# Performance work log

Measured on AMD Instinct MI355X. Metric: run time of the kernel, lower is better.

The kernel has to match this reference:

```python
import jax, jax.numpy as jnp
import numpy as np

D = 1024
H = 16
DH = D // H


def setup_inputs() -> dict:
    key = jax.random.key(0)
    ks = jax.random.split(key, 9)
    s = 1.0 / np.sqrt(D)
    return {
        "x": jax.random.normal(ks[0], (4, 2048, D), dtype=jnp.float32),
        "wq": jax.random.uniform(ks[1], (D, D), jnp.float32, -s, s),
        "bq": jax.random.uniform(ks[2], (D,), jnp.float32, -s, s),
        "wk": jax.random.uniform(ks[3], (D, D), jnp.float32, -s, s),
        "bk": jax.random.uniform(ks[4], (D,), jnp.float32, -s, s),
        "wv": jax.random.uniform(ks[5], (D, D), jnp.float32, -s, s),
        "bv": jax.random.uniform(ks[6], (D,), jnp.float32, -s, s),
        "wo": jax.random.uniform(ks[7], (D, D), jnp.float32, -s, s),
        "bo": jax.random.uniform(ks[8], (D,), jnp.float32, -s, s),
    }


def reference(x, wq, bq, wk, bk, wv, bv, wo, bo):
    B, S, _ = x.shape
    # projections + split heads: [B, S, D] -> [B, H, S, Dh]
    def split(t):
        return t.reshape(B, S, H, DH).transpose(0, 2, 1, 3)
    q = split(x @ wq + bq)
    k = split(x @ wk + bk)
    v = split(x @ wv + bv)
    scale = 1.0 / jnp.sqrt(jnp.float32(DH))
    scores = jnp.einsum("bhqd,bhkd->bhqk", q, k) * scale  # [B,H,S,S]
    att = jax.nn.softmax(scores, axis=-1)
    out = jnp.einsum("bhqk,bhkd->bhqd", att, v)  # [B,H,S,Dh]
    out = out.transpose(0, 2, 1, 3).reshape(B, S, D)
    return out @ wo + bo
```

## Files before the change

### kernel.cpp

```cpp
#include <hip/hip_runtime.h>
#include <stdint.h>

typedef float f32x4 __attribute__((ext_vector_type(4)));
typedef __bf16 bf16x8 __attribute__((ext_vector_type(8)));
typedef unsigned short ushort_t;
typedef ushort_t ushortx8 __attribute__((ext_vector_type(8)));
typedef ushort_t ushortx4 __attribute__((ext_vector_type(4)));

#define DEV static __device__ __forceinline__

DEV ushort_t f2bf(float f) {
  union { float f; uint32_t u; } v; v.f = f;
  uint32_t u = v.u;
  return (ushort_t)((u + 0x7FFFu + ((u >> 16) & 1u)) >> 16);
}

DEV uint32_t pkbf(float a, float b) {
  __bf16 x = (__bf16)a, y = (__bf16)b;
  return (uint32_t)__builtin_bit_cast(unsigned short, x) |
         ((uint32_t)__builtin_bit_cast(unsigned short, y) << 16);
}

DEV void cp16(const void* g, void* l) {
  __builtin_amdgcn_global_load_lds((const __attribute__((address_space(1))) unsigned int*)g,
                                   (__attribute__((address_space(3))) unsigned int*)l,
                                   16, 0, 0);
}

DEV f32x4 mfma16(bf16x8 a, bf16x8 b, f32x4 c) {
  return __builtin_amdgcn_mfma_f32_16x16x32_bf16(a, b, c, 0, 0, 0);
}

__global__ __launch_bounds__(256) void k_prep(
    const float* __restrict__ x, ushort_t* __restrict__ xb,
    const float* __restrict__ wq, const float* __restrict__ wk,
    const float* __restrict__ wv, const float* __restrict__ wo,
    ushort_t* __restrict__ wqkvT, ushort_t* __restrict__ woT) {
  __shared__ float tile[32][33];
  int b = blockIdx.x;
  if (b < 4096) {
    size_t idx = ((size_t)b * 256 + threadIdx.x) * 8;
    const float4* src = (const float4*)(x + idx);
    float4 a = src[0], c = src[1];
    ushortx8 o;
    o[0] = f2bf(a.x); o[1] = f2bf(a.y); o[2] = f2bf(a.z); o[3] = f2bf(a.w);
    o[4] = f2bf(c.x); o[5] = f2bf(c.y); o[6] = f2bf(c.z); o[7] = f2bf(c.w);
    *(ushortx8*)(xb + idx) = o;
  } else {
    int t = b - 4096;
    int which = t >> 10;
    const float* src = (which == 0) ? wq : (which == 1) ? wk : (which == 2) ? wv : wo;
    ushort_t* dst = (which == 0) ? wqkvT
                    : (which == 1) ? wqkvT + 1024 * 1024
                    : (which == 2) ? wqkvT + 2 * 1024 * 1024
                                   : woT;
    int tt = t & 1023;
    int c0 = (tt & 31) * 32, r0 = (tt >> 5) * 32;
    int tx = threadIdx.x & 31, ty = threadIdx.x >> 5;
#pragma unroll
    for (int i = ty; i < 32; i += 8)
      tile[i][tx] = src[(size_t)(r0 + i) * 1024 + c0 + tx];
    __syncthreads();
#pragma unroll
    for (int i = ty; i < 32; i += 8)
      dst[(size_t)(c0 + i) * 1024 + r0 + tx] = f2bf(tile[tx][i]);
  }
}

__global__ __launch_bounds__(256) void k_transpose_v(const ushort_t* __restrict__ vw,
                                                     ushort_t* __restrict__ vtw) {
  __shared__ ushort_t t[64][72];
  int tid = threadIdx.x;
  int bh = blockIdx.y, s0 = blockIdx.x * 64;
#pragma unroll
  for (int n = 0; n < 2; ++n) {
    int row = (tid >> 3) + n * 32, ch = (tid & 7) * 8;
    *(ushortx8*)&t[row][ch] =
        *(const ushortx8*)&vw[((size_t)bh * 2048 + s0 + row) * 64 + ch];
  }
  __syncthreads();
#pragma unroll
  for (int n = 0; n < 2; ++n) {
    int dh = (tid >> 3) + n * 32, sc = (tid & 7) * 8;
    ushortx8 o;
#pragma unroll
    for (int k = 0; k < 8; ++k) o[k] = t[sc + k][dh];
    *(ushortx8*)&vtw[((size_t)bh * 64 + dh) * 2048 + s0 + sc] = o;
  }
}

template <int MODE>
__global__ __launch_bounds__(256, 2) void k_gemm(
    const ushort_t* __restrict__ A, const ushort_t* __restrict__ Bt,
    const float* __restrict__ b0, const float* __restrict__ b1,
    const float* __restrict__ b2, ushort_t* __restrict__ qw,
    ushort_t* __restrict__ kw, ushort_t* __restrict__ vw,
    float* __restrict__ outf) {
  const int K = 1024;
  __shared__ ushort_t As[128 * 32];
  __shared__ ushort_t Bs[128 * 32];
  int tid = threadIdx.x;
  int w = tid >> 6, lane = tid & 63, l16 = lane & 15, lg = lane >> 4;
  int m0 = blockIdx.x * 128, n0 = blockIdx.y * 128;
  int wm = (w >> 1) * 64, wn = (w & 1) * 64;
  f32x4 acc[4][4] = {};

  const ushort_t* Ag = A + (size_t)(m0 + (tid >> 2)) * K + (tid & 3) * 8;
  const ushort_t* Bg = Bt + (size_t)(n0 + (tid >> 2)) * K + (tid & 3) * 8;

  for (int k0 = 0; k0 < K; k0 += 32) {
    cp16(Ag + k0, As + w * 512);
    cp16(Ag + k0 + 64 * K, As + 2048 + w * 512);
    cp16(Bg + k0, Bs + w * 512);
    cp16(Bg + k0 + 64 * K, Bs + 2048 + w * 512);
    __syncthreads();
    bf16x8 af[4], bfr[4];
#pragma unroll
    for (int i = 0; i < 4; ++i)
      af[i] = *(const bf16x8*)&As[(wm + i * 16 + l16) * 32 + lg * 8];
#pragma unroll
    for (int j = 0; j < 4; ++j)
      bfr[j] = *(const bf16x8*)&Bs[(wn + j * 16 + l16) * 32 + lg * 8];
#pragma unroll
    for (int i = 0; i < 4; ++i)
#pragma unroll
      for (int j = 0; j < 4; ++j)
        acc[i][j] = mfma16(af[i], bfr[j], acc[i][j]);
    __syncthreads();
  }

  if (MODE == 0) {
    const float QSCALE = 0.18033688011112042f;
    int p = m0 >> 10;
    const float* bias = (p == 0) ? b0 : (p == 1) ? b1 : b2;
    ushort_t* dst = (p == 0) ? qw : (p == 1) ? kw : vw;
    float qs = (p == 0) ? QSCALE : 1.0f;
    int cbase = m0 & 1023;
#pragma unroll
    for (int i = 0; i < 4; ++i) {
      int oc = cbase + wm + i * 16 + lg * 4;
      int h = oc >> 6, dh0 = oc & 63;
      float4 bb = *(const float4*)&bias[oc];
#pragma unroll
      for (int j = 0; j < 4; ++j) {
        int tok = n0 + wn + j * 16 + l16;
        size_t base =
            ((size_t)((tok >> 11) * 16 + h) * 2048 + (tok & 2047)) * 64 + dh0;
        ushortx4 pk;
        pk[0] = f2bf((acc[i][j][0] + bb.x) * qs);
        pk[1] = f2bf((acc[i][j][1] + bb.y) * qs);
        pk[2] = f2bf((acc[i][j][2] + bb.z) * qs);
        pk[3] = f2bf((acc[i][j][3] + bb.w) * qs);
        *(ushortx4*)&dst[base] = pk;
      }
    }
  } else {
#pragma unroll
    for (int j = 0; j < 4; ++j) {
      int col = n0 + wn + j * 16 + l16;
      float bb = b0[col];
#pragma unroll
      for (int i = 0; i < 4; ++i) {
#pragma unroll
        for (int r = 0; r < 4; ++r) {
          int row = m0 + wm + i * 16 + lg * 4 + r;
          outf[(size_t)row * 1024 + col] = acc[i][j][r] + bb;
        }
      }
    }
  }
}

__global__ __launch_bounds__(512, 4) void k_attn(
    const ushort_t* __restrict__ qg, const ushort_t* __restrict__ kg,
    const ushort_t* __restrict__ vtg, ushort_t* __restrict__ att) {
  __shared__ ushort_t Ks[128 * 64];
  __shared__ ushort_t Vs[64 * 128];
  __shared__ ushort_t Ps[8][16 * 128];
  int tid = threadIdx.x;
  int w = tid >> 6, lane = tid & 63, l16 = lane & 15, lg = lane >> 4;
  int i = blockIdx.x;
  int bh = (i & 7) * 8 + ((i >> 3) & 7);
  int q0 = (i >> 6) * 256;
  const ushort_t* qh = qg + (size_t)bh * 2048 * 64;

  const ushort_t* kstage = kg + (size_t)bh * 2048 * 64 + (size_t)(tid >> 3) * 64 +
                           (size_t)(((tid & 7) ^ ((tid >> 3) & 7)) * 8);
  const ushort_t* vstage = vtg + (size_t)bh * 64 * 2048 + (size_t)(tid >> 4) * 2048 +
                           (size_t)(((tid & 15) ^ ((tid >> 4) & 15)) * 8);

  bf16x8 qf[2][2];
#pragma unroll
  for (int st = 0; st < 2; ++st)
#pragma unroll
    for (int ks = 0; ks < 2; ++ks)
      qf[st][ks] = *(const bf16x8*)(qh + (size_t)(q0 + w * 32 + st * 16 + l16) * 64 +
                                    ks * 32 + lg * 8);

  bf16x8 vone;
#pragma unroll
  for (int t = 0; t < 8; ++t) vone[t] = (__bf16)1.0f;

  f32x4 o[2][5] = {};

  for (int kb = 0; kb < 2048; kb += 128) {
    __syncthreads();
    cp16(kstage + (size_t)kb * 64, Ks + w * 512);
    cp16(kstage + (size_t)(kb + 64) * 64, Ks + 4096 + w * 512);
    cp16(vstage + kb, Vs + w * 512);
    cp16(vstage + kb + (size_t)32 * 2048, Vs + 4096 + w * 512);
    __syncthreads();

#pragma unroll
    for (int hf = 0; hf < 2; ++hf) {
      f32x4 sc[2][4] = {};
#pragma unroll
      for (int jt = 0; jt < 4; ++jt) {
        int row = hf * 64 + jt * 16 + l16;
        bf16x8 kf0 = *(const bf16x8*)&Ks[row * 64 + ((lg) ^ (l16 & 7)) * 8];
        bf16x8 kf1 = *(const bf16x8*)&Ks[row * 64 + ((lg + 4) ^ (l16 & 7)) * 8];
        sc[0][jt] = mfma16(kf0, qf[0][0], sc[0][jt]);
        sc[0][jt] = mfma16(kf1, qf[0][1], sc[0][jt]);
        sc[1][jt] = mfma16(kf0, qf[1][0], sc[1][jt]);
        sc[1][jt] = mfma16(kf1, qf[1][1], sc[1][jt]);
      }
#pragma unroll
      for (int st = 0; st < 2; ++st)
#pragma unroll
        for (int jt = 0; jt < 4; ++jt) {
          float e0 = __builtin_amdgcn_exp2f(sc[st][jt][0]);
          float e1 = __builtin_amdgcn_exp2f(sc[st][jt][1]);
          float e2 = __builtin_amdgcn_exp2f(sc[st][jt][2]);
          float e3 = __builtin_amdgcn_exp2f(sc[st][jt][3]);
          uint32_t* dst =
              (uint32_t*)&Ps[w][l16 * 128 +
                                (((st * 8 + jt * 2 + (lg >> 1)) ^ l16) * 8) +
                                (lg & 1) * 4];
          dst[0] = pkbf(e0, e1);
          dst[1] = pkbf(e2, e3);
        }
#pragma unroll
      for (int ks = 0; ks < 2; ++ks) {
        int kk = hf * 2 + ks;
        bf16x8 pf0 =
            *(const bf16x8*)&Ps[w][l16 * 128 + (((ks * 4 + lg) ^ l16) * 8)];
        bf16x8 pf1 =
            *(const bf16x8*)&Ps[w][l16 * 128 + (((8 + ks * 4 + lg) ^ l16) * 8)];
        o[0][4] = mfma16(pf0, vone, o[0][4]);
        o[1][4] = mfma16(pf1, vone, o[1][4]);
#pragma unroll
        for (int dt = 0; dt < 4; ++dt) {
          int vrow = dt * 16 + l16;
          bf16x8 vf =
              *(const bf16x8*)&Vs[vrow * 128 + (((kk * 4 + lg) ^ l16) * 8)];
          o[0][dt] = mfma16(pf0, vf, o[0][dt]);
          o[1][dt] = mfma16(pf1, vf, o[1][dt]);
        }
      }
    }
  }

  int bi = bh >> 4, h = bh & 15;
#pragma unroll
  for (int st = 0; st < 2; ++st) {
    f32x4 inv;
#pragma unroll
    for (int r = 0; r < 4; ++r) inv[r] = __builtin_amdgcn_rcpf(o[st][4][r]);
#pragma unroll
    for (int dt = 0; dt < 4; ++dt)
#pragma unroll
      for (int r = 0; r < 4; ++r) {
        int srow = q0 + w * 32 + st * 16 + lg * 4 + r;
        int col = h * 64 + dt * 16 + l16;
        att[(size_t)(bi * 2048 + srow) * 1024 + col] = f2bf(o[st][dt][r] * inv[r]);
      }
  }
}

extern "C" void kernel_launch(void* const* d_in, const int* in_sizes, int n_in,
                              void* d_out, int out_size, void* d_ws, size_t ws_size,
                              hipStream_t stream) {
  const float* x = (const float*)d_in[0];
  const float* wq = (const float*)d_in[1];
  const float* bq = (const float*)d_in[2];
  const float* wk = (const float*)d_in[3];
  const float* bk = (const float*)d_in[4];
  const float* wv = (const float*)d_in[5];
  const float* bv = (const float*)d_in[6];
  const float* wo = (const float*)d_in[7];
  const float* bo = (const float*)d_in[8];
  float* out = (float*)d_out;

  char* ws = (char*)d_ws;
  ushort_t* xb = (ushort_t*)(ws);
  ushort_t* wqkvT = (ushort_t*)(ws + 16777216);
  ushort_t* woT = (ushort_t*)(ws + 23068672);
  ushort_t* qw = (ushort_t*)(ws + 25165824);
  ushort_t* kw = (ushort_t*)(ws + 41943040);
  ushort_t* vtw = (ushort_t*)(ws + 58720256);
  ushort_t* att = (ushort_t*)(ws + 75497472);
  ushort_t* vw = att;

  k_prep<<<dim3(8192), dim3(256), 0, stream>>>(x, xb, wq, wk, wv, wo, wqkvT, woT);

  k_gemm<0><<<dim3(24, 64), dim3(256), 0, stream>>>(
      wqkvT, xb, bq, bk, bv, qw, kw, vw, nullptr);

  k_transpose_v<<<dim3(32, 64), dim3(256), 0, stream>>>(vw, vtw);

  k_attn<<<dim3(512), dim3(512), 0, stream>>>(qw, kw, vtw, att);

  k_gemm<1><<<dim3(64, 8), dim3(256), 0, stream>>>(
      att, woT, bo, nullptr, nullptr, nullptr, nullptr, nullptr, out);
}
```

Before: 294.0 us.

## Replace QKV projection GEMM with 256x256-tile double-buffered pipelined kernel

Adds a new QKV projection kernel that uses 256x256 tiles with 512 threads, 128KB of dynamic LDS holding double-buffered A/B stages, and XOR-swizzled LDS rows. Global-to-LDS copies for the next K slice are interleaved between MFMA phases, using explicit waitcnt, barriers and setprio. The goal is to raise arithmetic intensity and hide load latency compared with the old 128x128 single-buffer GEMM. The trade-off is only 384 blocks at low occupancy, plus a hipFuncSetAttribute call on every launch. The output GEMM is simplified to MODE 1 only.

```diff
diff --git a/kernel.cpp b/kernel.cpp
--- a/kernel.cpp
+++ b/kernel.cpp
@@ -89,13 +89,167 @@
   }
 }
 
+__global__ __launch_bounds__(512, 2) void k_gemm256(
+    const ushort_t* __restrict__ A, const ushort_t* __restrict__ Bt,
+    const float* __restrict__ b0, const float* __restrict__ b1,
+    const float* __restrict__ b2, ushort_t* __restrict__ qw,
+    ushort_t* __restrict__ kw, ushort_t* __restrict__ vw) {
+  extern __shared__ ushort_t lds[];
+  ushort_t* As = lds;
+  ushort_t* Bs = lds + 32768;
+  const int K = 1024, NT = 16;
+  int tid = threadIdx.x;
+  int w = tid >> 6, lane = tid & 63, l16 = lane & 15, lg = lane >> 4;
+  int wr = w >> 2, wc = w & 3;
+  int m0 = blockIdx.x * 256, n0 = blockIdx.y * 256;
+
+  const ushort_t* Asrc = A + (size_t)(m0 + w * 8 + (lane >> 3)) * K +
+                         (size_t)(((lane & 7) ^ (lane >> 3)) * 8);
+  const ushort_t* Bsrc = Bt + (size_t)(n0 + w * 8 + (lane >> 3)) * K +
+                         (size_t)(((lane & 7) ^ (lane >> 3)) * 8);
+
+  f32x4 acc[8][4] = {};
+  bf16x8 a[4][2], b[4][2];
+  const int aRow = wr * 128 + l16, bRow = wc * 64 + l16, rsw = l16 & 7;
+
+#pragma unroll
+  for (int s = 0; s < 4; ++s)
+    cp16(Asrc + (size_t)s * 64 * K, As + s * 4096 + w * 512);
+#pragma unroll
+  for (int s = 0; s < 4; ++s)
+    cp16(Bsrc + (size_t)s * 64 * K, Bs + s * 4096 + w * 512);
+  cp16(Asrc + 64, As + 16384 + w * 512);
+  cp16(Asrc + (size_t)65536 + 64, As + 16384 + 4096 + w * 512);
+  asm volatile("s_waitcnt vmcnt(2)" ::: "memory");
+  __builtin_amdgcn_s_barrier();
+
+  for (int t = 0; t < NT; ++t) {
+    int cur = t & 1, nxt = cur ^ 1;
+    ushort_t* AsC = As + cur * 16384;
+    ushort_t* BsC = Bs + cur * 16384;
+    ushort_t* AsN = As + nxt * 16384;
+    ushort_t* BsN = Bs + nxt * 16384;
+    const ushort_t* An = Asrc + (size_t)(t + 1) * 64;
+    const ushort_t* Bn = Bsrc + (size_t)(t + 1) * 64;
+
+#pragma unroll
+    for (int i2 = 0; i2 < 4; ++i2)
+#pragma unroll
+      for (int ks = 0; ks < 2; ++ks)
+        a[i2][ks] = *(const bf16x8*)&AsC[(aRow + i2 * 16) * 64 +
+                                         (((ks << 2) | lg) ^ rsw) * 8];
+#pragma unroll
+    for (int j2 = 0; j2 < 2; ++j2)
+#pragma unroll
+      for (int ks = 0; ks < 2; ++ks)
+        b[j2][ks] = *(const bf16x8*)&BsC[(bRow + j2 * 16) * 64 +
+                                         (((ks << 2) | lg) ^ rsw) * 8];
+    cp16(An + (size_t)2 * 65536, AsN + 2 * 4096 + w * 512);
+    cp16(An + (size_t)3 * 65536, AsN + 3 * 4096 + w * 512);
+    __builtin_amdgcn_s_barrier();
+    asm volatile("s_waitcnt lgkmcnt(0)" ::: "memory");
+    __builtin_amdgcn_s_setprio(1);
+#pragma unroll
+    for (int i2 = 0; i2 < 4; ++i2)
+#pragma unroll
+      for (int j2 = 0; j2 < 2; ++j2)
+#pragma unroll
+        for (int ks = 0; ks < 2; ++ks)
+          acc[i2][j2] = mfma16(a[i2][ks], b[j2][ks], acc[i2][j2]);
+    __builtin_amdgcn_s_setprio(0);
+    __builtin_amdgcn_s_barrier();
+
+#pragma unroll
+    for (int j2 = 2; j2 < 4; ++j2)
+#pragma unroll
+      for (int ks = 0; ks < 2; ++ks)
+        b[j2][ks] = *(const bf16x8*)&BsC[(bRow + j2 * 16) * 64 +
+                                         (((ks << 2) | lg) ^ rsw) * 8];
+    cp16(Bn, BsN + w * 512);
+    cp16(Bn + (size_t)65536, BsN + 4096 + w * 512);
+    __builtin_amdgcn_s_barrier();
+    asm volatile("s_waitcnt lgkmcnt(0)" ::: "memory");
+    __builtin_amdgcn_s_setprio(1);
+#pragma unroll
+    for (int i2 = 0; i2 < 4; ++i2)
+#pragma unroll
+      for (int j2 = 2; j2 < 4; ++j2)
+#pragma unroll
+        for (int ks = 0; ks < 2; ++ks)
+          acc[i2][j2] = mfma16(a[i2][ks], b[j2][ks], acc[i2][j2]);
+    __builtin_amdgcn_s_setprio(0);
+    __builtin_amdgcn_s_barrier();
+
+#pragma unroll
+    for (int i2 = 0; i2 < 4; ++i2)
+#pragma unroll
+      for (int ks = 0; ks < 2; ++ks)
+        a[i2][ks] = *(const bf16x8*)&AsC[(aRow + (4 + i2) * 16) * 64 +
+                                         (((ks << 2) | lg) ^ rsw) * 8];
+    cp16(Bn + (size_t)2 * 65536, BsN + 2 * 4096 + w * 512);
+    cp16(Bn + (size_t)3 * 65536, BsN + 3 * 4096 + w * 512);
+    __builtin_amdgcn_s_barrier();
+    asm volatile("s_waitcnt lgkmcnt(0)" ::: "memory");
+    __builtin_amdgcn_s_setprio(1);
+#pragma unroll
+    for (int i2 = 0; i2 < 4; ++i2)
+#pragma unroll
+      for (int j2 = 2; j2 < 4; ++j2)
+#pragma unroll
+        for (int ks = 0; ks < 2; ++ks)
+          acc[4 + i2][j2] = mfma16(a[i2][ks], b[j2][ks], acc[4 + i2][j2]);
+    __builtin_amdgcn_s_setprio(0);
+    __builtin_amdgcn_s_barrier();
+
+    {
+      const ushort_t* A2 = Asrc + (size_t)(t + 2) * 64;
+      cp16(A2, AsC + w * 512);
+      cp16(A2 + (size_t)65536, AsC + 4096 + w * 512);
+    }
+    asm volatile("s_waitcnt vmcnt(2)" ::: "memory");
+    __builtin_amdgcn_s_barrier();
+    __builtin_amdgcn_s_setprio(1);
+#pragma unroll
+    for (int i2 = 0; i2 < 4; ++i2)
+#pragma unroll
+      for (int j2 = 0; j2 < 2; ++j2)
+#pragma unroll
+        for (int ks = 0; ks < 2; ++ks)
+          acc[4 + i2][j2] = mfma16(a[i2][ks], b[j2][ks], acc[4 + i2][j2]);
+    __builtin_amdgcn_s_setprio(0);
+    __builtin_amdgcn_s_barrier();
+  }
+
+  const float QSCALE = 0.18033688011112042f;
+  int p = blockIdx.x >> 2;
+  const float* bias = (p == 0) ? b0 : (p == 1) ? b1 : b2;
+  ushort_t* dst = (p == 0) ? qw : (p == 1) ? kw : vw;
+  float qs = (p == 0) ? QSCALE : 1.0f;
+  int cbase = (m0 & 1023) + wr * 128;
+#pragma unroll
+  for (int i = 0; i < 8; ++i) {
+    int oc = cbase + i * 16 + lg * 4;
+    int h = oc >> 6, dh0 = oc & 63;
+    float4 bb = *(const float4*)&bias[oc];
+#pragma unroll
+    for (int j = 0; j < 4; ++j) {
+      int tok = n0 + wc * 64 + j * 16 + l16;
+      size_t base =
+          ((size_t)((tok >> 11) * 16 + h) * 2048 + (tok & 2047)) * 64 + dh0;
+      ushortx4 pk;
+      pk[0] = f2bf((acc[i][j][0] + bb.x) * qs);
+      pk[1] = f2bf((acc[i][j][1] + bb.y) * qs);
+      pk[2] = f2bf((acc[i][j][2] + bb.z) * qs);
+      pk[3] = f2bf((acc[i][j][3] + bb.w) * qs);
+      *(ushortx4*)&dst[base] = pk;
+    }
+  }
+}
+
 template <int MODE>
 __global__ __launch_bounds__(256, 2) void k_gemm(
     const ushort_t* __restrict__ A, const ushort_t* __restrict__ Bt,
-    const float* __restrict__ b0, const float* __restrict__ b1,
-    const float* __restrict__ b2, ushort_t* __restrict__ qw,
-    ushort_t* __restrict__ kw, ushort_t* __restrict__ vw,
-    float* __restrict__ outf) {
+    const float* __restrict__ b0, float* __restrict__ outf) {
   const int K = 1024;
   __shared__ ushort_t As[128 * 32];
   __shared__ ushort_t Bs[128 * 32];
@@ -129,43 +283,16 @@
     __syncthreads();
   }
 
-  if (MODE == 0) {
-    const float QSCALE = 0.18033688011112042f;
-    int p = m0 >> 10;
-    const float* bias = (p == 0) ? b0 : (p == 1) ? b1 : b2;
-    ushort_t* dst = (p == 0) ? qw : (p == 1) ? kw : vw;
-    float qs = (p == 0) ? QSCALE : 1.0f;
-    int cbase = m0 & 1023;
+#pragma unroll
+  for (int j = 0; j < 4; ++j) {
+    int col = n0 + wn + j * 16 + l16;
+    float bb = b0[col];
 #pragma unroll
     for (int i = 0; i < 4; ++i) {
-      int oc = cbase + wm + i * 16 + lg * 4;
-      int h = oc >> 6, dh0 = oc & 63;
-      float4 bb = *(const float4*)&bias[oc];
-#pragma unroll
-      for (int j = 0; j < 4; ++j) {
-        int tok = n0 + wn + j * 16 + l16;
-        size_t base =
-            ((size_t)((tok >> 11) * 16 + h) * 2048 + (tok & 2047)) * 64 + dh0;
-        ushortx4 pk;
-        pk[0] = f2bf((acc[i][j][0] + bb.x) * qs);
-        pk[1] = f2bf((acc[i][j][1] + bb.y) * qs);
-        pk[2] = f2bf((acc[i][j][2] + bb.z) * qs);
-        pk[3] = f2bf((acc[i][j][3] + bb.w) * qs);
-        *(ushortx4*)&dst[base] = pk;
-      }
-    }
-  } else {
-#pragma unroll
-    for (int j = 0; j < 4; ++j) {
-      int col = n0 + wn + j * 16 + l16;
-      float bb = b0[col];
-#pragma unroll
-      for (int i = 0; i < 4; ++i) {
-#pragma unroll
-        for (int r = 0; r < 4; ++r) {
-          int row = m0 + wm + i * 16 + lg * 4 + r;
-          outf[(size_t)row * 1024 + col] = acc[i][j][r] + bb;
-        }
+#pragma unroll
+      for (int r = 0; r < 4; ++r) {
+        int row = m0 + wm + i * 16 + lg * 4 + r;
+        outf[(size_t)row * 1024 + col] = acc[i][j][r] + bb;
       }
     }
   }
@@ -303,13 +430,15 @@
 
   k_prep<<<dim3(8192), dim3(256), 0, stream>>>(x, xb, wq, wk, wv, wo, wqkvT, woT);
 
-  k_gemm<0><<<dim3(24, 64), dim3(256), 0, stream>>>(
-      wqkvT, xb, bq, bk, bv, qw, kw, vw, nullptr);
+  const int GEMM0_LDS = 131072;
+  hipFuncSetAttribute(reinterpret_cast<const void*>(&k_gemm256),
+                      hipFuncAttributeMaxDynamicSharedMemorySize, GEMM0_LDS);
+  k_gemm256<<<dim3(12, 32), dim3(512), GEMM0_LDS, stream>>>(
+      wqkvT, xb, bq, bk, bv, qw, kw, vw);
 
   k_transpose_v<<<dim3(32, 64), dim3(256), 0, stream>>>(vw, vtw);
 
   k_attn<<<dim3(512), dim3(512), 0, stream>>>(qw, kw, vtw, att);
 
-  k_gemm<1><<<dim3(64, 8), dim3(256), 0, stream>>>(
-      att, woT, bo, nullptr, nullptr, nullptr, nullptr, nullptr, out);
-}
+  k_gemm<1><<<dim3(64, 8), dim3(256), 0, stream>>>(att, woT, bo, out);
+}
```

Measured after the change: 276.6 us. 5.9% less time.
